# Performance work log

Measured on AMD Instinct MI355X. Metric: run time of the kernel, lower is better.

Reference implementation:

```python
import jax, jax.numpy as jnp
import numpy as np

B, T, C = 4, 2048, 2048
N_HEAD = 16
HEAD_DIM = C // N_HEAD  # 128
ROPE_BASE = 10000.0


def rope_cache(dim, seq_len, base=ROPE_BASE):
    inv_freq = 1.0 / (base ** (jnp.arange(0, dim, 2, dtype=jnp.float32) / dim))
    t = jnp.arange(seq_len, dtype=jnp.float32)
    freqs = jnp.outer(t, inv_freq)  # [T, dim//2]
    return jnp.cos(freqs), jnp.sin(freqs)


def apply_rope(q, k, cos, sin):
    # q, k: [B, H, T, D], interleaved-pair rotation
    q1, q2 = q[..., 0::2], q[..., 1::2]
    k1, k2 = k[..., 0::2], k[..., 1::2]
    c = cos[None, None, :, :]
    s = sin[None, None, :, :]
    q_rot = jnp.stack([q1 * c - q2 * s, q1 * s + q2 * c], axis=-1).reshape(q.shape)
    k_rot = jnp.stack([k1 * c - k2 * s, k1 * s + k2 * c], axis=-1).reshape(k.shape)
    return q_rot, k_rot


def setup_inputs() -> dict:
    key = jax.random.key(0)
    k1, k2, k3 = jax.random.split(key, 3)
    x = jax.random.normal(k1, (B, T, C), dtype=jnp.float32)
    W_attn = jax.random.normal(k2, (3 * C, C), dtype=jnp.float32) * (1.0 / np.sqrt(C))
    W_proj = jax.random.normal(k3, (C, C), dtype=jnp.float32) * (1.0 / np.sqrt(C))
    return {"x": x, "W_attn": W_attn, "W_proj": W_proj}


def reference(x, W_attn, W_proj):
    Bx, Tx, Cx = x.shape
    qkv = jnp.einsum('btc,fc->btf', x, W_attn)  # [B, T, 3C]
    q, k, v = jnp.split(qkv, 3, axis=-1)
    # [B, H, T, D]
    q = q.reshape(Bx, Tx, N_HEAD, HEAD_DIM).transpose(0, 2, 1, 3)
    k = k.reshape(Bx, Tx, N_HEAD, HEAD_DIM).transpose(0, 2, 1, 3)
    v = v.reshape(Bx, Tx, N_HEAD, HEAD_DIM).transpose(0, 2, 1, 3)
    cos, sin = rope_cache(HEAD_DIM, Tx)
    q, k = apply_rope(q, k, cos, sin)
    scale = 1.0 / np.sqrt(HEAD_DIM)
    scores = jnp.einsum('bhqd,bhkd->bhqk', q, k) * scale
    causal = jnp.tril(jnp.ones((Tx, Tx), dtype=bool))
    scores = jnp.where(causal[None, None, :, :], scores, jnp.finfo(scores.dtype).min)
    attn = jax.nn.softmax(scores, axis=-1)
    y = jnp.einsum('bhqk,bhkd->bhqd', attn, v)
    y = y.transpose(0, 2, 1, 3).reshape(Bx, Tx, Cx)
    return jnp.einsum('btc,fc->btf', y, W_proj)
```

## Files before the change

kernel.cpp:

```cpp
#include <hip/hip_runtime.h>
#include <stdint.h>

#define TT 2048
#define CC 2048
#define NHEAD 16
#define HD 128
#define NB 4
#define MTOT (NB*TT)
#define KD 2048
#define NT 32

typedef __attribute__((ext_vector_type(8))) short bf16x8;
typedef __attribute__((ext_vector_type(4))) float f32x4;
typedef __attribute__((ext_vector_type(16))) float f32x16;
typedef __attribute__((ext_vector_type(4))) unsigned u32x4;

__device__ __forceinline__ unsigned short f2bf(float f) {
  unsigned u = __float_as_uint(f);
  u += 0x7FFF + ((u >> 16) & 1);
  return (unsigned short)(u >> 16);
}
__device__ __forceinline__ float bf2f(unsigned short h) {
  return __uint_as_float(((unsigned)h) << 16);
}

__device__ __forceinline__ void gl_lds16(const unsigned short* g, short* l) {
  __builtin_amdgcn_global_load_lds(
      (const __attribute__((address_space(1))) void*)(g),
      (__attribute__((address_space(3))) void*)(l), 16, 0, 0);
}

#define MFMA16(a, b, c) __builtin_amdgcn_mfma_f32_16x16x32_bf16((a), (b), (c), 0, 0, 0)
#define MFMA32(a, b, c) __builtin_amdgcn_mfma_f32_32x32x16_bf16((a), (b), (c), 0, 0, 0)

#define PRE_MFMA() do { \
  __builtin_amdgcn_s_barrier(); \
  asm volatile("s_waitcnt lgkmcnt(0)" ::: "memory"); \
  __builtin_amdgcn_s_setprio(1); \
} while(0)
#define POST_MFMA() do { \
  __builtin_amdgcn_s_setprio(0); \
  __builtin_amdgcn_s_barrier(); \
  __builtin_amdgcn_sched_barrier(0); \
} while(0)

__global__ void k_f2b(const float* __restrict__ in, unsigned short* __restrict__ out, int n4) {
  int i = blockIdx.x * 256 + threadIdx.x;
  if (i >= n4) return;
  float4 v = reinterpret_cast<const float4*>(in)[i];
  ushort4 o;
  o.x = f2bf(v.x); o.y = f2bf(v.y); o.z = f2bf(v.z); o.w = f2bf(v.w);
  reinterpret_cast<ushort4*>(out)[i] = o;
}

__global__ void k_rope_tab(float* __restrict__ tab) {
  int t = blockIdx.x, i = threadIdx.x;
  double inv = exp2(-(double)i * (13.287712379549449062 / 64.0));
  double ang = (double)t * inv;
  tab[(t*64 + i)*2 + 0] = (float)cos(ang);
  tab[(t*64 + i)*2 + 1] = (float)sin(ang);
}

__device__ __forceinline__ void gemm256_core(
    const unsigned short* __restrict__ Ag,
    const unsigned short* __restrict__ Bg,
    int m0, int n0, short* lds, f32x4 (&acc)[8][4])
{
  const int tid = threadIdx.x;
  const int wid = tid >> 6, lane = tid & 63;
  const int wm = wid >> 2, wn = wid & 3;
  const int r15 = lane & 15, hi4 = lane >> 4;
  const int srow = wid*8 + (lane >> 3);
  const int schunk = (lane & 7) ^ (lane >> 3);

  const f32x4 fz = {0.f, 0.f, 0.f, 0.f};
#pragma unroll
  for (int i = 0; i < 8; i++)
#pragma unroll
    for (int j = 0; j < 4; j++) acc[i][j] = fz;

  int aoff0[8];
#pragma unroll
  for (int mi = 0; mi < 8; mi++) {
    int row = wm*128 + mi*16 + r15;
    aoff0[mi] = row*64 + ((hi4 ^ (row & 7))*8);
  }
  int boff0[4];
#pragma unroll
  for (int ni = 0; ni < 4; ni++) {
    int row = wn*64 + ni*16 + r15;
    boff0[ni] = row*64 + ((hi4 ^ (row & 7))*8);
  }

#define STAGE(G, L, GROW0, KT) do { \
    gl_lds16((G) + (size_t)((GROW0) + srow)*KD + (KT) + schunk*8, (L) + wid*512); \
    gl_lds16((G) + (size_t)((GROW0) + 64 + srow)*KD + (KT) + schunk*8, (L) + 4096 + wid*512); \
  } while(0)

  STAGE(Ag, lds,                        m0,       0);
  STAGE(Ag, lds + 8192,                 m0 + 128, 0);
  STAGE(Bg, lds + 32768,                n0,       0);
  STAGE(Bg, lds + 32768 + 8192,         n0 + 128, 0);
  STAGE(Bg, lds + 32768 + 16384,        n0,       64);
  STAGE(Bg, lds + 32768 + 16384 + 8192, n0 + 128, 64);
  asm volatile("s_waitcnt vmcnt(4)" ::: "memory");
  __builtin_amdgcn_s_barrier();
  __builtin_amdgcn_sched_barrier(0);

#pragma unroll 1
  for (int t = 0; t < NT; t++) {
    const int db = t & 1;
    short* Ab = lds + db*16384;
    short* Bb = lds + 32768 + db*16384;
    short* An = lds + (db ^ 1)*16384;
    const int kt = t*64;
    const bool stA = (t < NT - 1);
    const bool stB = (t < NT - 2);

    bf16x8 a[8], b[4][2];
#pragma unroll
    for (int mi = 0; mi < 8; mi++)
      a[mi] = *reinterpret_cast<const bf16x8*>(Ab + aoff0[mi]);
#pragma unroll
    for (int ni = 0; ni < 4; ni++) {
      b[ni][0] = *reinterpret_cast<const bf16x8*>(Bb + boff0[ni]);
      b[ni][1] = *reinterpret_cast<const bf16x8*>(Bb + (boff0[ni] ^ 32));
    }
    if (stA) {
      STAGE(Ag, An,        m0,       kt + 64);
      STAGE(Ag, An + 8192, m0 + 128, kt + 64);
    }
    PRE_MFMA();
#pragma unroll
    for (int mi = 0; mi < 8; mi++)
#pragma unroll
      for (int ni = 0; ni < 4; ni++)
        acc[mi][ni] = MFMA16(a[mi], b[ni][0], acc[mi][ni]);
    POST_MFMA();

#pragma unroll
    for (int mi = 0; mi < 8; mi++)
      a[mi] = *reinterpret_cast<const bf16x8*>(Ab + (aoff0[mi] ^ 32));
    if (stB) {
      STAGE(Bg, Bb,        n0,       kt + 128);
      STAGE(Bg, Bb + 8192, n0 + 128, kt + 128);
    }
    if (t >= NT - 2) asm volatile("s_waitcnt vmcnt(0)" ::: "memory");
    else             asm volatile("s_waitcnt vmcnt(4)" ::: "memory");
    PRE_MFMA();
#pragma unroll
    for (int mi = 0; mi < 8; mi++)
#pragma unroll
      for (int ni = 0; ni < 4; ni++)
        acc[mi][ni] = MFMA16(a[mi], b[ni][1], acc[mi][ni]);
    POST_MFMA();
  }
#undef STAGE
}

__global__ __launch_bounds__(512, 2) void k_qkv(
    const unsigned short* __restrict__ xb,
    const unsigned short* __restrict__ wab,
    const float* __restrict__ tab,
    unsigned short* __restrict__ qr,
    unsigned short* __restrict__ kr,
    unsigned short* __restrict__ vt)
{
  __shared__ __align__(16) short lds[65536];
  f32x4 acc[8][4];
  int bid = blockIdx.x;
  int xcd = bid & 7, idx = bid >> 3;
  int m0 = (xcd*4 + (idx & 3))*256;
  int n0 = (idx >> 2)*256;
  gemm256_core(xb, wab, m0, n0, lds, acc);

  int tid = threadIdx.x, wid = tid >> 6, lane = tid & 63;
  int wm = wid >> 2, wn = wid & 3, r15 = lane & 15, hi4 = lane >> 4;
  int nw0 = n0 + wn*64;
  int which = nw0 >> 11;
  int h = (nw0 & 2047) >> 7;
#pragma unroll
  for (int mi = 0; mi < 8; mi++) {
    int m_base = m0 + wm*128 + mi*16 + hi4*4;
    int b = m_base >> 11;
    int t0 = m_base & (TT - 1);
#pragma unroll
    for (int ni = 0; ni < 4; ni++) {
      int d = (nw0 & 127) + ni*16 + r15;
      if (which == 2) {
        ushort4 pv;
        pv.x = f2bf(acc[mi][ni][0]); pv.y = f2bf(acc[mi][ni][1]);
        pv.z = f2bf(acc[mi][ni][2]); pv.w = f2bf(acc[mi][ni][3]);
        *reinterpret_cast<ushort4*>(vt + ((size_t)((b*NHEAD + h)*HD + d))*TT + t0) = pv;
      } else {
        unsigned short* dst = (which == 0) ? qr : kr;
        size_t base = ((size_t)(b*NHEAD + h)*TT + t0)*HD + d;
        int j = d >> 1;
        bool odd = (d & 1);
#pragma unroll
        for (int r = 0; r < 4; r++) {
          float v = acc[mi][ni][r];
          float pv = __shfl_xor(v, 1);
          float2 cs = *reinterpret_cast<const float2*>(tab + ((size_t)(t0 + r)*64 + j)*2);
          float res = odd ? (pv*cs.y + v*cs.x) : (v*cs.x - pv*cs.y);
          dst[base + (size_t)r*HD] = f2bf(res);
        }
      }
    }
  }
}

__global__ __launch_bounds__(512, 2) void k_proj(
    const unsigned short* __restrict__ yb,
    const unsigned short* __restrict__ wpb,
    float* __restrict__ out)
{
  __shared__ __align__(16) short lds[65536];
  f32x4 acc[8][4];
  int bid = blockIdx.x;
  int xcd = bid & 7, idx = bid >> 3;
  int m0 = (xcd*4 + (idx & 3))*256;
  int n0 = (idx >> 2)*256;
  gemm256_core(yb, wpb, m0, n0, lds, acc);

  int tid = threadIdx.x, wid = tid >> 6, lane = tid & 63;
  int wm = wid >> 2, wn = wid & 3, r15 = lane & 15, hi4 = lane >> 4;
  int nw0 = n0 + wn*64;
#pragma unroll
  for (int mi = 0; mi < 8; mi++) {
    int m = m0 + wm*128 + mi*16 + hi4*4;
#pragma unroll
    for (int ni = 0; ni < 4; ni++) {
      int n = nw0 + ni*16 + r15;
#pragma unroll
      for (int r = 0; r < 4; r++)
        out[(size_t)(m + r)*CC + n] = acc[mi][ni][r];
    }
  }
}

__global__ __launch_bounds__(512, 1) void k_attn(
    const unsigned short* __restrict__ qr,
    const unsigned short* __restrict__ kr,
    const unsigned short* __restrict__ vt,
    unsigned short* __restrict__ yb)
{
  __shared__ __align__(16) short Ks[2][64*128];
  __shared__ __align__(16) short Vs[2][128*64];
  __shared__ float alds[8][32];
  int bid = blockIdx.x;
  int bh = bid & 63, pr = bid >> 6;
  int tid = threadIdx.x, w = tid >> 6, lane = tid & 63;
  int l31 = lane & 31, hi = lane >> 5;
  const unsigned short* qg = qr + (size_t)bh*TT*HD;
  const unsigned short* kg = kr + (size_t)bh*TT*HD;
  const unsigned short* vg = vt + (size_t)bh*HD*TT;
  const float scale = 0.08838834764831845f;
  int b = bh >> 4, h = bh & 15;

  int ksoff[2], vsoff[2];
#pragma unroll
  for (int i = 0; i < 2; i++) {
    int c = w*2 + i;
    int rK = c*4 + (lane >> 4);
    int cK = (lane & 15) ^ (rK & 7);
    ksoff[i] = rK*HD + cK*8;
    int dV = c*8 + (lane >> 3);
    int cV = (lane & 7) ^ (dV & 7);
    vsoff[i] = dV*TT + cV*8;
  }

#define STAGE_KV(BUF, KV0) do { \
    _Pragma("unroll") \
    for (int i_ = 0; i_ < 2; i_++) { \
      gl_lds16(kg + (size_t)(KV0)*HD + ksoff[i_], &Ks[BUF][(w*2 + i_)*512]); \
      gl_lds16(vg + (KV0) + vsoff[i_],            &Vs[BUF][(w*2 + i_)*512]); \
    } \
  } while(0)

#pragma unroll 1
  for (int ph = 0; ph < 2; ph++) {
    int qb = ph ? (7 - pr) : pr;
    int qlo = qb*256 + w*32;
    int qgi = qlo + l31;
    bf16x8 qf[8];
#pragma unroll
    for (int kk = 0; kk < 8; kk++)
      qf[kk] = *reinterpret_cast<const bf16x8*>(qg + (size_t)qgi*HD + kk*16 + hi*8);

    f32x16 ao[4];
#pragma unroll
    for (int dt = 0; dt < 4; dt++)
#pragma unroll
      for (int r = 0; r < 16; r++) ao[dt][r] = 0.f;
    float mrow = -3.0e38f, lsum = 0.f;
    int ntiles = 4*qb + 4;

    STAGE_KV(0, 0);
    __syncthreads();
    int cur = 0;

#pragma unroll 1
    for (int it = 0; it < ntiles; ++it) {
      int kv0 = it*64;
      if (it + 1 < ntiles) STAGE_KV(cur ^ 1, kv0 + 64);
      if (kv0 <= qlo + 31) {
        const short* Kc = Ks[cur];
        const short* Vc = Vs[cur];
        bool full = (kv0 + 63 <= qlo);
        f32x16 s0, s1;
#pragma unroll
        for (int r = 0; r < 16; r++) { s0[r] = 0.f; s1[r] = 0.f; }
        __builtin_amdgcn_s_setprio(1);
#pragma unroll
        for (int kk = 0; kk < 8; kk++) {
          int row0 = l31, row1 = 32 + l31;
          int ch0 = ((2*kk + hi) ^ (row0 & 7));
          int ch1 = ((2*kk + hi) ^ (row1 & 7));
          bf16x8 kf0 = *reinterpret_cast<const bf16x8*>((const char*)Kc + row0*256 + ch0*16);
          bf16x8 kf1 = *reinterpret_cast<const bf16x8*>((const char*)Kc + row1*256 + ch1*16);
          s0 = MFMA32(kf0, qf[kk], s0);
          s1 = MFMA32(kf1, qf[kk], s1);
        }
        __builtin_amdgcn_s_setprio(0);
        float p[32];
#pragma unroll
        for (int r = 0; r < 16; r++) {
          int kvl = (r & 3) + 8*(r >> 2) + 4*hi;
          float v0 = s0[r]*scale, v1 = s1[r]*scale;
          if (!full) {
            v0 = (kv0 + kvl      <= qgi) ? v0 : -3.0e38f;
            v1 = (kv0 + 32 + kvl <= qgi) ? v1 : -3.0e38f;
          }
          p[r] = v0; p[16 + r] = v1;
        }
        float t16[16];
#pragma unroll
        for (int i = 0; i < 16; i++) t16[i] = fmaxf(p[i], p[i + 16]);
#pragma unroll
        for (int i = 0; i < 8; i++) t16[i] = fmaxf(t16[i], t16[i + 8]);
#pragma unroll
        for (int i = 0; i < 4; i++) t16[i] = fmaxf(t16[i], t16[i + 4]);
        float mx = fmaxf(fmaxf(t16[0], t16[1]), fmaxf(t16[2], t16[3]));
        mx = fmaxf(mx, __shfl_xor(mx, 32));
        bool defer = __all(mx <= mrow + 8.f);
        if (!defer) {
          float mnew = fmaxf(mrow, mx);
          float alpha = __expf(mrow - mnew);
          mrow = mnew;
          lsum *= alpha;
          if (lane < 32) alds[w][lane] = alpha;
#pragma unroll
          for (int r = 0; r < 16; r++) {
            int ql = (r & 3) + 8*(r >> 2) + 4*hi;
            float av = alds[w][ql];
#pragma unroll
            for (int dt = 0; dt < 4; dt++) ao[dt][r] *= av;
          }
        }
#pragma unroll
        for (int i = 0; i < 32; i++) p[i] = __expf(p[i] - mrow);
#pragma unroll
        for (int i = 0; i < 16; i++) t16[i] = p[i] + p[i + 16];
#pragma unroll
        for (int i = 0; i < 8; i++) t16[i] = t16[i] + t16[i + 8];
#pragma unroll
        for (int i = 0; i < 4; i++) t16[i] = t16[i] + t16[i + 4];
        float rs = (t16[0] + t16[1]) + (t16[2] + t16[3]);
        rs += __shfl_xor(rs, 32);
        lsum += rs;
        bf16x8 pa[4];
#pragma unroll
        for (int ks = 0; ks < 4; ks++) {
          const int base = (ks >> 1)*16 + (ks & 1)*8;
          unsigned a0, a1, b0, b1;
          asm("v_cvt_pk_bf16_f32 %0, %1, %2" : "=v"(a0) : "v"(p[base + 0]), "v"(p[base + 1]));
          asm("v_cvt_pk_bf16_f32 %0, %1, %2" : "=v"(a1) : "v"(p[base + 2]), "v"(p[base + 3]));
          asm("v_cvt_pk_bf16_f32 %0, %1, %2" : "=v"(b0) : "v"(p[base + 4]), "v"(p[base + 5]));
          asm("v_cvt_pk_bf16_f32 %0, %1, %2" : "=v"(b1) : "v"(p[base + 6]), "v"(p[base + 7]));
          unsigned sa0 = (unsigned)__shfl_xor((int)a0, 32);
          unsigned sa1 = (unsigned)__shfl_xor((int)a1, 32);
          unsigned sb0 = (unsigned)__shfl_xor((int)b0, 32);
          unsigned sb1 = (unsigned)__shfl_xor((int)b1, 32);
          u32x4 pw;
          pw.x = hi ? sb0 : a0;
          pw.y = hi ? sb1 : a1;
          pw.z = hi ? b0 : sa0;
          pw.w = hi ? b1 : sa1;
          pa[ks] = __builtin_bit_cast(bf16x8, pw);
        }
        __builtin_amdgcn_s_setprio(1);
#pragma unroll
        for (int dt = 0; dt < 4; dt++) {
          int d = dt*32 + l31;
#pragma unroll
          for (int ks = 0; ks < 4; ks++) {
            int ch = ((2*ks + hi) ^ (d & 7));
            bf16x8 vf = *reinterpret_cast<const bf16x8*>((const char*)Vc + d*128 + ch*16);
            ao[dt] = MFMA32(pa[ks], vf, ao[dt]);
          }
        }
        __builtin_amdgcn_s_setprio(0);
      }
      __syncthreads();
      cur ^= 1;
    }
    if (lane < 32) alds[w][lane] = 1.0f / lsum;
#pragma unroll
    for (int r = 0; r < 16; r++) {
      int ql = (r & 3) + 8*(r >> 2) + 4*hi;
      float lv = alds[w][ql];
      int t = qlo + ql;
      size_t base = ((size_t)b*TT + t)*CC + h*HD + l31;
#pragma unroll
      for (int dt = 0; dt < 4; dt++)
        yb[base + dt*32] = f2bf(ao[dt][r] * lv);
    }
    __syncthreads();
  }
#undef STAGE_KV
}

extern "C" void kernel_launch(void* const* d_in, const int* in_sizes, int n_in,
                              void* d_out, int out_size, void* d_ws, size_t ws_size,
                              hipStream_t stream) {
  const float* x  = (const float*)d_in[0];
  const float* wa = (const float*)d_in[1];
  const float* wp = (const float*)d_in[2];
  float* out = (float*)d_out;
  char* ws = (char*)d_ws;
  size_t off = 0;
  unsigned short* xb  = (unsigned short*)(ws + off); off += (size_t)MTOT*CC*2;
  unsigned short* wab = (unsigned short*)(ws + off); off += (size_t)3*CC*CC*2;
  unsigned short* wpb = (unsigned short*)(ws + off); off += (size_t)CC*CC*2;
  unsigned short* qr  = (unsigned short*)(ws + off); off += (size_t)MTOT*CC*2;
  unsigned short* kr  = (unsigned short*)(ws + off); off += (size_t)MTOT*CC*2;
  unsigned short* vt  = (unsigned short*)(ws + off); off += (size_t)MTOT*CC*2;
  unsigned short* yb  = (unsigned short*)(ws + off); off += (size_t)MTOT*CC*2;
  float* tab          = (float*)(ws + off);          off += (size_t)TT*64*2*4;

  k_f2b<<<dim3(16384), dim3(256), 0, stream>>>(x,  xb,  MTOT*CC/4);
  k_f2b<<<dim3(12288), dim3(256), 0, stream>>>(wa, wab, 3*CC*CC/4);
  k_f2b<<<dim3(4096),  dim3(256), 0, stream>>>(wp, wpb, CC*CC/4);
  k_rope_tab<<<dim3(TT), dim3(64), 0, stream>>>(tab);
  k_qkv<<<dim3(768), dim3(512), 0, stream>>>(xb, wab, tab, qr, kr, vt);
  k_attn<<<dim3(256), dim3(512), 0, stream>>>(qr, kr, vt, yb);
  k_proj<<<dim3(256), dim3(512), 0, stream>>>(yb, wpb, out);
}
```

Before: 406.2 us.

## Load GEMM B operand directly into registers and halve LDS staging

The shared GEMM core stops staging the weight (B) tile through LDS. Each wave now prefetches its B fragments straight from global memory into registers one k-step ahead, and only A is double-buffered in LDS. Per-MFMA-block barriers are dropped in favour of a single barrier per iteration, and the LDS allocation shrinks by half. This reduces LDS traffic and synchronisation, but B is loaded redundantly across waves with scattered row accesses, and register pressure goes up.

Result: slower. 579.3 us (+42.6%).

```diff
diff --git a/kernel.cpp b/kernel.cpp
--- a/kernel.cpp
+++ b/kernel.cpp
@@ -32,17 +32,6 @@
 
 #define MFMA16(a, b, c) __builtin_amdgcn_mfma_f32_16x16x32_bf16((a), (b), (c), 0, 0, 0)
 #define MFMA32(a, b, c) __builtin_amdgcn_mfma_f32_32x32x16_bf16((a), (b), (c), 0, 0, 0)
-
-#define PRE_MFMA() do { \
-  __builtin_amdgcn_s_barrier(); \
-  asm volatile("s_waitcnt lgkmcnt(0)" ::: "memory"); \
-  __builtin_amdgcn_s_setprio(1); \
-} while(0)
-#define POST_MFMA() do { \
-  __builtin_amdgcn_s_setprio(0); \
-  __builtin_amdgcn_s_barrier(); \
-  __builtin_amdgcn_sched_barrier(0); \
-} while(0)
 
 __global__ void k_f2b(const float* __restrict__ in, unsigned short* __restrict__ out, int n4) {
   int i = blockIdx.x * 256 + threadIdx.x;
@@ -85,75 +74,71 @@
     int row = wm*128 + mi*16 + r15;
     aoff0[mi] = row*64 + ((hi4 ^ (row & 7))*8);
   }
-  int boff0[4];
+  const unsigned short* bbase[4];
+#pragma unroll
+  for (int ni = 0; ni < 4; ni++)
+    bbase[ni] = Bg + (size_t)(n0 + wn*64 + ni*16 + r15)*KD + hi4*8;
+
+#define STAGE(L, GROW0, KT) do { \
+    gl_lds16(Ag + (size_t)((GROW0) + srow)*KD + (KT) + schunk*8, (L) + wid*512); \
+    gl_lds16(Ag + (size_t)((GROW0) + 64 + srow)*KD + (KT) + schunk*8, (L) + 4096 + wid*512); \
+  } while(0)
+
+  bf16x8 b[4][2], bn[4][2];
+  STAGE(lds,        m0,       0);
+  STAGE(lds + 8192, m0 + 128, 0);
 #pragma unroll
   for (int ni = 0; ni < 4; ni++) {
-    int row = wn*64 + ni*16 + r15;
-    boff0[ni] = row*64 + ((hi4 ^ (row & 7))*8);
-  }
-
-#define STAGE(G, L, GROW0, KT) do { \
-    gl_lds16((G) + (size_t)((GROW0) + srow)*KD + (KT) + schunk*8, (L) + wid*512); \
-    gl_lds16((G) + (size_t)((GROW0) + 64 + srow)*KD + (KT) + schunk*8, (L) + 4096 + wid*512); \
-  } while(0)
-
-  STAGE(Ag, lds,                        m0,       0);
-  STAGE(Ag, lds + 8192,                 m0 + 128, 0);
-  STAGE(Bg, lds + 32768,                n0,       0);
-  STAGE(Bg, lds + 32768 + 8192,         n0 + 128, 0);
-  STAGE(Bg, lds + 32768 + 16384,        n0,       64);
-  STAGE(Bg, lds + 32768 + 16384 + 8192, n0 + 128, 64);
-  asm volatile("s_waitcnt vmcnt(4)" ::: "memory");
+    b[ni][0] = *reinterpret_cast<const bf16x8*>(bbase[ni]);
+    b[ni][1] = *reinterpret_cast<const bf16x8*>(bbase[ni] + 32);
+  }
+  asm volatile("s_waitcnt vmcnt(0)" ::: "memory");
   __builtin_amdgcn_s_barrier();
   __builtin_amdgcn_sched_barrier(0);
 
 #pragma unroll 1
   for (int t = 0; t < NT; t++) {
-    const int db = t & 1;
-    short* Ab = lds + db*16384;
-    short* Bb = lds + 32768 + db*16384;
-    short* An = lds + (db ^ 1)*16384;
+    short* Ab = lds + (t & 1)*16384;
+    short* An = lds + ((t & 1) ^ 1)*16384;
     const int kt = t*64;
     const bool stA = (t < NT - 1);
-    const bool stB = (t < NT - 2);
-
-    bf16x8 a[8], b[4][2];
+
+    if (stA) {
+      STAGE(An,        m0,       kt + 64);
+      STAGE(An + 8192, m0 + 128, kt + 64);
+#pragma unroll
+      for (int ni = 0; ni < 4; ni++) {
+        bn[ni][0] = *reinterpret_cast<const bf16x8*>(bbase[ni] + kt + 64);
+        bn[ni][1] = *reinterpret_cast<const bf16x8*>(bbase[ni] + kt + 96);
+      }
+    }
+    bf16x8 a[8];
 #pragma unroll
     for (int mi = 0; mi < 8; mi++)
       a[mi] = *reinterpret_cast<const bf16x8*>(Ab + aoff0[mi]);
-#pragma unroll
-    for (int ni = 0; ni < 4; ni++) {
-      b[ni][0] = *reinterpret_cast<const bf16x8*>(Bb + boff0[ni]);
-      b[ni][1] = *reinterpret_cast<const bf16x8*>(Bb + (boff0[ni] ^ 32));
-    }
-    if (stA) {
-      STAGE(Ag, An,        m0,       kt + 64);
-      STAGE(Ag, An + 8192, m0 + 128, kt + 64);
-    }
-    PRE_MFMA();
+    __builtin_amdgcn_s_setprio(1);
 #pragma unroll
     for (int mi = 0; mi < 8; mi++)
 #pragma unroll
       for (int ni = 0; ni < 4; ni++)
         acc[mi][ni] = MFMA16(a[mi], b[ni][0], acc[mi][ni]);
-    POST_MFMA();
-
+    __builtin_amdgcn_s_setprio(0);
 #pragma unroll
     for (int mi = 0; mi < 8; mi++)
       a[mi] = *reinterpret_cast<const bf16x8*>(Ab + (aoff0[mi] ^ 32));
-    if (stB) {
-      STAGE(Bg, Bb,        n0,       kt + 128);
-      STAGE(Bg, Bb + 8192, n0 + 128, kt + 128);
-    }
-    if (t >= NT - 2) asm volatile("s_waitcnt vmcnt(0)" ::: "memory");
-    else             asm volatile("s_waitcnt vmcnt(4)" ::: "memory");
-    PRE_MFMA();
+    __builtin_amdgcn_s_setprio(1);
 #pragma unroll
     for (int mi = 0; mi < 8; mi++)
 #pragma unroll
       for (int ni = 0; ni < 4; ni++)
         acc[mi][ni] = MFMA16(a[mi], b[ni][1], acc[mi][ni]);
-    POST_MFMA();
+    __builtin_amdgcn_s_setprio(0);
+    if (stA) asm volatile("s_waitcnt vmcnt(8)" ::: "memory");
+    else     asm volatile("s_waitcnt vmcnt(0)" ::: "memory");
+    __builtin_amdgcn_s_barrier();
+    __builtin_amdgcn_sched_barrier(0);
+#pragma unroll
+    for (int ni = 0; ni < 4; ni++) { b[ni][0] = bn[ni][0]; b[ni][1] = bn[ni][1]; }
   }
 #undef STAGE
 }
@@ -166,7 +151,7 @@
     unsigned short* __restrict__ kr,
     unsigned short* __restrict__ vt)
 {
-  __shared__ __align__(16) short lds[65536];
+  __shared__ __align__(16) short lds[32768];
   f32x4 acc[8][4];
   int bid = blockIdx.x;
   int xcd = bid & 7, idx = bid >> 3;
@@ -215,7 +200,7 @@
     const unsigned short* __restrict__ wpb,
     float* __restrict__ out)
 {
-  __shared__ __align__(16) short lds[65536];
+  __shared__ __align__(16) short lds[32768];
   f32x4 acc[8][4];
   int bid = blockIdx.x;
   int xcd = bid & 7, idx = bid >> 3;
```
